# Performance work log

Hardware: AMD Instinct MI355X
Metric: run time of the kernel (lower is better)

## Reference

```python
import jax, jax.numpy as jnp
import numpy as np

N_NODES = 100000
F_IN = 128


def gcn_conv(x, W, b, src, dst, num_nodes):
    """PyG GCNConv: add self-loops, symmetric deg^-1/2 normalization,
    aggregate then linear (equivalently linear then aggregate)."""
    h = x @ W  # [N, F_out]
    # self-loops
    loop = jnp.arange(num_nodes, dtype=src.dtype)
    s = jnp.concatenate([src, loop])
    d = jnp.concatenate([dst, loop])
    ones = jnp.ones(s.shape[0], dtype=x.dtype)
    deg = jax.ops.segment_sum(ones, d, num_segments=num_nodes)  # in-degree w/ self-loops
    dinv = jnp.where(deg > 0, jax.lax.rsqrt(deg), 0.0)
    norm = dinv[s] * dinv[d]  # [E+N]
    msg = h[s] * norm[:, None]  # gather + scale
    out = jax.ops.segment_sum(msg, d, num_segments=num_nodes)  # scatter-add
    return out + b


def setup_inputs() -> dict:
    key = jax.random.key(0)
    k1, k2, k3, k4 = jax.random.split(key, 4)
    x = jax.random.normal(k1, (N_NODES, F_IN), dtype=jnp.float32)
    edge_index = jax.random.randint(k2, (2, 600000), 0, N_NODES, dtype=jnp.int64)
    # GCNConv weights (glorot-ish scale) and zero biases
    W1 = jax.random.normal(k3, (F_IN, F_IN), dtype=jnp.float32) / np.sqrt(F_IN)
    b1 = jnp.zeros((F_IN,), dtype=jnp.float32)
    W2 = jax.random.normal(k4, (F_IN, 2 * F_IN), dtype=jnp.float32) / np.sqrt(F_IN)
    b2 = jnp.zeros((2 * F_IN,), dtype=jnp.float32)
    return {"x": x, "edge_index": edge_index, "W1": W1, "b1": b1, "W2": W2, "b2": b2}


def reference(x, edge_index, W1, b1, W2, b2):
    src, dst = edge_index[0], edge_index[1]
    n = x.shape[0]
    h = gcn_conv(x, W1, b1, src, dst, n)
    h = jax.nn.relu(h)  # dropout is identity in eval mode
    h = gcn_conv(h, W2, b2, src, dst, n)
    h = jax.nn.relu(h)
    return jnp.mean(h, axis=0)  # [2*F_IN]
```

## Files before the change

### kernel.cpp

```cpp
#include <hip/hip_runtime.h>


typedef __attribute__((ext_vector_type(8))) short short8;
typedef __attribute__((ext_vector_type(4))) float f32x4;

__device__ __forceinline__ float b2f(unsigned short u) {
    union { unsigned int i; float f; } c;
    c.i = ((unsigned int)u) << 16;
    return c.f;
}
__device__ __forceinline__ unsigned short f2b(float x) {
    union { float f; unsigned int i; } c;
    c.f = x;
    unsigned int r = c.i + 0x7FFFu + ((c.i >> 16) & 1u);
    return (unsigned short)(r >> 16);
}

__device__ __forceinline__ int edge_idx(const void* ei, int is64, int which,
                                        int E, int e) {
    if (is64) return (int)((const long long*)ei)[(size_t)which * E + e];
    return ((const int*)ei)[(size_t)which * E + e];
}

__global__ void k_init(const int* __restrict__ ei, int E, int* __restrict__ counts,
                       int* __restrict__ flag, int N) {
    int i = blockIdx.x * 256 + threadIdx.x;
    if (i < N) counts[i] = 0;
    if (blockIdx.x == 0) {
        __shared__ int anyv[4];
        int t = threadIdx.x;
        int v = 0;
#pragma unroll
        for (int r = 0; r < 4; ++r) {
            long long k = (long long)(t * 4 + r) * E >> 10;
            v |= ei[2 * (int)k + 1];
        }
        unsigned long long m = __ballot(v != 0);
        if ((t & 63) == 0) anyv[t >> 6] = (m != 0ull) ? 1 : 0;
        __syncthreads();
        if (t == 0) flag[0] = anyv[0] | anyv[1] | anyv[2] | anyv[3];
    }
}

__global__ void k_count(const void* __restrict__ ei, const int* __restrict__ flag,
                        int* __restrict__ counts, int E) {
    int e = blockIdx.x * 256 + threadIdx.x;
    if (e >= E) return;
    int is64 = (*flag == 0);
    int d = edge_idx(ei, is64, 1, E, e);
    atomicAdd(&counts[d], 1);
}

__global__ void k_scan1(const int* __restrict__ counts, int* __restrict__ offs,
                        int* __restrict__ blockSums, float* __restrict__ dinv,
                        int n) {
    __shared__ int tmp[256];
    int t = threadIdx.x;
    int i = blockIdx.x * 256 + t;
    int my = (i < n) ? counts[i] : 0;
    if (i < n) dinv[i] = rsqrtf(1.0f + (float)my);
    tmp[t] = my;
    __syncthreads();
    for (int off = 1; off < 256; off <<= 1) {
        int v = (t >= off) ? tmp[t - off] : 0;
        __syncthreads();
        tmp[t] += v;
        __syncthreads();
    }
    if (i < n) offs[i] = tmp[t] - my;
    if (t == 255) blockSums[blockIdx.x] = tmp[255];
}

__global__ void k_scan2(int* __restrict__ blockSums, int nb) {
    __shared__ int tmp[512];
    __shared__ int carry;
    int t = threadIdx.x;
    if (t == 0) carry = 0;
    __syncthreads();
    for (int base = 0; base < nb; base += 512) {
        int i = base + t;
        int my = (i < nb) ? blockSums[i] : 0;
        tmp[t] = my;
        __syncthreads();
        for (int off = 1; off < 512; off <<= 1) {
            int v = (t >= off) ? tmp[t - off] : 0;
            __syncthreads();
            tmp[t] += v;
            __syncthreads();
        }
        if (i < nb) blockSums[i] = carry + tmp[t] - my;
        __syncthreads();
        if (t == 0) carry += tmp[511];
        __syncthreads();
    }
}

__global__ void k_scan3(int* __restrict__ offs, const int* __restrict__ blockSums,
                        int* __restrict__ cursor, int n) {
    int i = blockIdx.x * 256 + threadIdx.x;
    if (i < n) {
        int o = offs[i] + blockSums[blockIdx.x];
        offs[i] = o;
        cursor[i] = o;
    }
}

__global__ void k_fill_csr(const void* __restrict__ ei, const int* __restrict__ flag,
                           const float* __restrict__ dinv, int* __restrict__ cursor,
                           int2* __restrict__ csr2, int E) {
    int e = blockIdx.x * 256 + threadIdx.x;
    if (e >= E) return;
    int is64 = (*flag == 0);
    int s = edge_idx(ei, is64, 0, E, e);
    int d = edge_idx(ei, is64, 1, E, e);
    int pos = atomicAdd(&cursor[d], 1);
    csr2[pos] = make_int2(s, __float_as_int(dinv[s] * dinv[d]));
}

__global__ void k_cvt_x(const float* __restrict__ x, unsigned short* __restrict__ xb,
                        int n4) {
    int i = blockIdx.x * 256 + threadIdx.x;
    if (i >= n4) return;
    float4 v = reinterpret_cast<const float4*>(x)[i];
    ushort4 o;
    o.x = f2b(v.x); o.y = f2b(v.y); o.z = f2b(v.z); o.w = f2b(v.w);
    reinterpret_cast<ushort4*>(xb)[i] = o;
}

__global__ void k_cvt_w(const float* __restrict__ W1, const float* __restrict__ W2,
                        unsigned short* __restrict__ wt1,
                        unsigned short* __restrict__ wt2) {
    int idx = blockIdx.x * 256 + threadIdx.x;
    if (idx < 128 * 128) {
        int k = idx >> 7, n = idx & 127;
        wt1[(size_t)n * 128 + k] = f2b(W1[idx]);
    } else if (idx < 128 * 128 + 128 * 256) {
        int i2 = idx - 128 * 128;
        int k = i2 >> 8, n = i2 & 255;
        wt2[(size_t)n * 128 + k] = f2b(W2[i2]);
    }
}

template <int CHUNK>
__global__ __launch_bounds__(256) void k_gather_b(const unsigned short* __restrict__ h,
                                                  const float* __restrict__ dinv,
                                                  const int* __restrict__ offs,
                                                  const int* __restrict__ counts,
                                                  const int2* __restrict__ csr2,
                                                  unsigned short* __restrict__ g,
                                                  int N) {
    const int wid = threadIdx.x >> 6;
    const int slot = (threadIdx.x >> 4) & 3;
    const int l16 = threadIdx.x & 15;
    const short8* h8 = reinterpret_cast<const short8*>(h);
    const int start = blockIdx.x * (CHUNK * 4);

    for (int i = 0; i < CHUNK; ++i) {
        const int node = start + i * 4 + wid;
        if (node >= N) continue;
        float a[8] = {0.f, 0.f, 0.f, 0.f, 0.f, 0.f, 0.f, 0.f};
        const size_t rowu = (size_t)node * 16 + l16;
        if (slot == 0) {
            const float dd = dinv[node];
            const float w0 = dd * dd;
            short8 sv = h8[rowu];
#pragma unroll
            for (int j = 0; j < 8; ++j) a[j] = b2f((unsigned short)sv[j]) * w0;
        }
        const int beg = offs[node], cnt = counts[node];
        for (int e = slot; e < cnt; e += 4) {
            int2 p = csr2[beg + e];
            short8 v = h8[(size_t)p.x * 16 + l16];
            float w = __int_as_float(p.y);
#pragma unroll
            for (int j = 0; j < 8; ++j)
                a[j] = fmaf(b2f((unsigned short)v[j]), w, a[j]);
        }
#pragma unroll
        for (int j = 0; j < 8; ++j) {
            a[j] += __shfl_xor(a[j], 16);
            a[j] += __shfl_xor(a[j], 32);
        }
        if (slot == 0) {
            short8 o;
#pragma unroll
            for (int j = 0; j < 8; ++j) o[j] = (short)f2b(a[j]);
            reinterpret_cast<short8*>(g)[rowu] = o;
        }
    }
}

template <int KOUT, bool REDUCE, int CHUNK>
__global__ __launch_bounds__(256) void k_mgemm(const unsigned short* __restrict__ A,
                                               const unsigned short* __restrict__ WT,
                                               const float* __restrict__ bias,
                                               unsigned short* __restrict__ C,
                                               float* __restrict__ partials, int N) {
    constexpr int NFW = KOUT / 64;
    const int tid = threadIdx.x;
    const int wave = tid >> 6, lane = tid & 63;
    const int l15 = lane & 15, lg = lane >> 4;
    const int colbase = wave * (KOUT / 4);

    short8 breg[NFW][4];
    float bv[NFW];
#pragma unroll
    for (int nf = 0; nf < NFW; ++nf) {
        int col = colbase + nf * 16 + l15;
        bv[nf] = bias[col];
#pragma unroll
        for (int kk = 0; kk < 4; ++kk)
            breg[nf][kk] = *reinterpret_cast<const short8*>(
                WT + (size_t)col * 128 + kk * 32 + lg * 8);
    }

    float psum[NFW];
#pragma unroll
    for (int nf = 0; nf < NFW; ++nf) psum[nf] = 0.f;

    const int NT = (N + 15) / 16;
    const int t0 = blockIdx.x * CHUNK;
    const int tend = (t0 + CHUNK < NT) ? t0 + CHUNK : NT;

#pragma unroll 2
    for (int t = t0; t < tend; ++t) {
        const int rows = t * 16;
        const int arow = rows + l15;
        short8 a[4];
        const bool rv = arow < N;
#pragma unroll
        for (int kk = 0; kk < 4; ++kk)
            a[kk] = rv ? *reinterpret_cast<const short8*>(
                             A + (size_t)arow * 128 + kk * 32 + lg * 8)
                       : (short8){0, 0, 0, 0, 0, 0, 0, 0};

        f32x4 acc[NFW];
#pragma unroll
        for (int nf = 0; nf < NFW; ++nf) acc[nf] = (f32x4){0.f, 0.f, 0.f, 0.f};
#pragma unroll
        for (int kk = 0; kk < 4; ++kk)
#pragma unroll
            for (int nf = 0; nf < NFW; ++nf)
                acc[nf] = __builtin_amdgcn_mfma_f32_16x16x32_bf16(
                    a[kk], breg[nf][kk], acc[nf], 0, 0, 0);

        if (!REDUCE) {
#pragma unroll
            for (int nf = 0; nf < NFW; ++nf) {
                int col = colbase + nf * 16 + l15;
#pragma unroll
                for (int r = 0; r < 4; ++r) {
                    int rr = rows + lg * 4 + r;
                    if (rr < N)
                        C[(size_t)rr * KOUT + col] =
                            f2b(fmaxf(acc[nf][r] + bv[nf], 0.f));
                }
            }
        } else {
#pragma unroll
            for (int nf = 0; nf < NFW; ++nf) {
#pragma unroll
                for (int r = 0; r < 4; ++r) {
                    int rr = rows + lg * 4 + r;
                    if (rr < N) psum[nf] += fmaxf(acc[nf][r] + bv[nf], 0.f);
                }
            }
        }
    }

    if (REDUCE) {
#pragma unroll
        for (int nf = 0; nf < NFW; ++nf) {
            float s = psum[nf];
            s += __shfl_xor(s, 16);
            s += __shfl_xor(s, 32);
            if (lg == 0)
                partials[(size_t)blockIdx.x * KOUT + colbase + nf * 16 + l15] = s;
        }
    }
}

__global__ void k_reduce1(const float* __restrict__ partials, float* __restrict__ p2,
                          int NB) {
    int c = threadIdx.x;
    float sum = 0.f;
    for (int r = blockIdx.x; r < NB; r += 16)
        sum += partials[(size_t)r * 256 + c];
    p2[blockIdx.x * 256 + c] = sum;
}

__global__ void k_reduce2(const float* __restrict__ p2, float* __restrict__ out,
                          float invN) {
    int c = threadIdx.x;
    float sum = 0.f;
#pragma unroll
    for (int b = 0; b < 16; ++b) sum += p2[b * 256 + c];
    out[c] = sum * invN;
}

extern "C" void kernel_launch(void* const* d_in, const int* in_sizes, int n_in,
                              void* d_out, int out_size, void* d_ws, size_t ws_size,
                              hipStream_t stream) {
    const float* x  = (const float*)d_in[0];
    const void*  ei = d_in[1];
    const float* W1 = (const float*)d_in[2];
    const float* b1 = (const float*)d_in[3];
    const float* W2 = (const float*)d_in[4];
    const float* b2 = (const float*)d_in[5];
    float* out = (float*)d_out;

    const int N = in_sizes[0] / 128;
    const int E = in_sizes[1] / 2;
    const int nb = (N + 255) / 256;
    constexpr int GCHUNK = 4;
    constexpr int MCHUNK = 8;
    const int NT = (N + 15) / 16;
    const int NBLK = (NT + MCHUNK - 1) / MCHUNK;
    const int GBLK = (N + GCHUNK * 4 - 1) / (GCHUNK * 4);

    char* ws = (char*)d_ws;
    size_t off = 0;
    auto alloc = [&](size_t bytes) {
        char* p = ws + off;
        off += (bytes + 255) & ~(size_t)255;
        return p;
    };
    int*            flag      = (int*)alloc(4);
    int*            counts    = (int*)alloc((size_t)N * 4);
    int*            offs      = (int*)alloc((size_t)N * 4);
    int*            cursor    = (int*)alloc((size_t)N * 4);
    int*            blockSums = (int*)alloc((size_t)nb * 4);
    float*          dinv      = (float*)alloc((size_t)N * 4);
    int2*           csr2      = (int2*)alloc((size_t)E * 8);
    float*          partials  = (float*)alloc((size_t)NBLK * 256 * 4);
    float*          p2        = (float*)alloc((size_t)16 * 256 * 4);
    unsigned short* wt1       = (unsigned short*)alloc((size_t)128 * 128 * 2);
    unsigned short* wt2       = (unsigned short*)alloc((size_t)256 * 128 * 2);
    unsigned short* xb        = (unsigned short*)alloc((size_t)N * 128 * 2);
    unsigned short* g1        = (unsigned short*)alloc((size_t)N * 128 * 2);
    unsigned short* a1r       = (unsigned short*)alloc((size_t)N * 128 * 2);
    unsigned short* g2        = xb;

    k_init<<<nb, 256, 0, stream>>>((const int*)ei, E, counts, flag, N);
    k_count<<<(E + 255) / 256, 256, 0, stream>>>(ei, flag, counts, E);
    k_scan1<<<nb, 256, 0, stream>>>(counts, offs, blockSums, dinv, N);
    k_scan2<<<1, 512, 0, stream>>>(blockSums, nb);
    k_scan3<<<nb, 256, 0, stream>>>(offs, blockSums, cursor, N);
    k_fill_csr<<<(E + 255) / 256, 256, 0, stream>>>(ei, flag, dinv, cursor, csr2, E);

    k_cvt_x<<<(N * 32 + 255) / 256, 256, 0, stream>>>(x, xb, N * 32);
    k_cvt_w<<<(128 * 384 + 255) / 256, 256, 0, stream>>>(W1, W2, wt1, wt2);

    k_gather_b<GCHUNK><<<GBLK, 256, 0, stream>>>(xb, dinv, offs, counts, csr2, g1, N);
    k_mgemm<128, false, MCHUNK><<<NBLK, 256, 0, stream>>>(g1, wt1, b1, a1r, nullptr, N);

    k_gather_b<GCHUNK><<<GBLK, 256, 0, stream>>>(a1r, dinv, offs, counts, csr2, g2, N);
    k_mgemm<256, true, MCHUNK><<<NBLK, 256, 0, stream>>>(g2, wt2, b2, nullptr, partials, N);
    k_reduce1<<<16, 256, 0, stream>>>(partials, p2, NBLK);
    k_reduce2<<<1, 256, 0, stream>>>(p2, out, 1.0f / (float)N);
}
```

Baseline: 240.1 us.

## Restructure gather so each 16-lane group streams a contiguous node range with prefetch

```diff
diff --git a/kernel.cpp b/kernel.cpp
--- a/kernel.cpp
+++ b/kernel.cpp
@@ -142,50 +142,55 @@
 }
 
 template <int CHUNK>
-__global__ __launch_bounds__(256) void k_gather_b(const unsigned short* __restrict__ h,
+__global__ __launch_bounds__(256) void k_gather_s(const unsigned short* __restrict__ h,
                                                   const float* __restrict__ dinv,
                                                   const int* __restrict__ offs,
                                                   const int* __restrict__ counts,
                                                   const int2* __restrict__ csr2,
                                                   unsigned short* __restrict__ g,
-                                                  int N) {
-    const int wid = threadIdx.x >> 6;
-    const int slot = (threadIdx.x >> 4) & 3;
-    const int l16 = threadIdx.x & 15;
+                                                  int N, int E) {
+    const int grp = threadIdx.x >> 4, l16 = threadIdx.x & 15;
     const short8* h8 = reinterpret_cast<const short8*>(h);
-    const int start = blockIdx.x * (CHUNK * 4);
-
-    for (int i = 0; i < CHUNK; ++i) {
-        const int node = start + i * 4 + wid;
-        if (node >= N) continue;
-        float a[8] = {0.f, 0.f, 0.f, 0.f, 0.f, 0.f, 0.f, 0.f};
-        const size_t rowu = (size_t)node * 16 + l16;
-        if (slot == 0) {
-            const float dd = dinv[node];
+    int n = (blockIdx.x * 16 + grp) * CHUNK;
+    if (n >= N) return;
+    const int gend = (n + CHUNK < N) ? n + CHUNK : N;
+    int e = offs[n];
+    int eEnd = e + counts[n];
+    const int endAll = (gend < N) ? offs[gend] : E;
+
+    float dd = dinv[n];
+    short8 selfv = h8[(size_t)n * 16 + l16];
+    float a[8] = {0.f, 0.f, 0.f, 0.f, 0.f, 0.f, 0.f, 0.f};
+
+    int2 p = make_int2(0, 0);
+    short8 v = (short8){0, 0, 0, 0, 0, 0, 0, 0};
+    if (e < endAll) { p = csr2[e]; v = h8[(size_t)p.x * 16 + l16]; }
+
+    for (;;) {
+        if (e == eEnd) {
             const float w0 = dd * dd;
-            short8 sv = h8[rowu];
-#pragma unroll
-            for (int j = 0; j < 8; ++j) a[j] = b2f((unsigned short)sv[j]) * w0;
-        }
-        const int beg = offs[node], cnt = counts[node];
-        for (int e = slot; e < cnt; e += 4) {
-            int2 p = csr2[beg + e];
-            short8 v = h8[(size_t)p.x * 16 + l16];
-            float w = __int_as_float(p.y);
+            short8 o;
+#pragma unroll
+            for (int j = 0; j < 8; ++j) {
+                float t = fmaf(b2f((unsigned short)selfv[j]), w0, a[j]);
+                o[j] = (short)f2b(t);
+            }
+            reinterpret_cast<short8*>(g)[(size_t)n * 16 + l16] = o;
+            if (++n == gend) break;
+            dd = dinv[n];
+            selfv = h8[(size_t)n * 16 + l16];
+            eEnd += counts[n];
+#pragma unroll
+            for (int j = 0; j < 8; ++j) a[j] = 0.f;
+        } else {
+            const int en = e + 1;
+            int2 pn = p; short8 vn = v;
+            if (en < endAll) { pn = csr2[en]; vn = h8[(size_t)pn.x * 16 + l16]; }
+            const float w = __int_as_float(p.y);
 #pragma unroll
             for (int j = 0; j < 8; ++j)
                 a[j] = fmaf(b2f((unsigned short)v[j]), w, a[j]);
-        }
-#pragma unroll
-        for (int j = 0; j < 8; ++j) {
-            a[j] += __shfl_xor(a[j], 16);
-            a[j] += __shfl_xor(a[j], 32);
-        }
-        if (slot == 0) {
-            short8 o;
-#pragma unroll
-            for (int j = 0; j < 8; ++j) o[j] = (short)f2b(a[j]);
-            reinterpret_cast<short8*>(g)[rowu] = o;
+            p = pn; v = vn; e = en;
         }
     }
 }
@@ -316,7 +321,7 @@
     constexpr int MCHUNK = 8;
     const int NT = (N + 15) / 16;
     const int NBLK = (NT + MCHUNK - 1) / MCHUNK;
-    const int GBLK = (N + GCHUNK * 4 - 1) / (GCHUNK * 4);
+    const int GBLK = (N + GCHUNK * 16 - 1) / (GCHUNK * 16);
 
     char* ws = (char*)d_ws;
     size_t off = 0;
@@ -351,10 +356,10 @@
     k_cvt_x<<<(N * 32 + 255) / 256, 256, 0, stream>>>(x, xb, N * 32);
     k_cvt_w<<<(128 * 384 + 255) / 256, 256, 0, stream>>>(W1, W2, wt1, wt2);
 
-    k_gather_b<GCHUNK><<<GBLK, 256, 0, stream>>>(xb, dinv, offs, counts, csr2, g1, N);
+    k_gather_s<GCHUNK><<<GBLK, 256, 0, stream>>>(xb, dinv, offs, counts, csr2, g1, N, E);
     k_mgemm<128, false, MCHUNK><<<NBLK, 256, 0, stream>>>(g1, wt1, b1, a1r, nullptr, N);
 
-    k_gather_b<GCHUNK><<<GBLK, 256, 0, stream>>>(a1r, dinv, offs, counts, csr2, g2, N);
+    k_gather_s<GCHUNK><<<GBLK, 256, 0, stream>>>(a1r, dinv, offs, counts, csr2, g2, N, E);
     k_mgemm<256, true, MCHUNK><<<NBLK, 256, 0, stream>>>(g2, wt2, b2, nullptr, partials, N);
     k_reduce1<<<16, 256, 0, stream>>>(partials, p2, NBLK);
     k_reduce2<<<1, 256, 0, stream>>>(p2, out, 1.0f / (float)N);
```

Measured after the change: 233.3 us. 1.03x faster.

## Fuse neighbor aggregation into MFMA GEMM via swizzled LDS tiles

Applied to the files above, without the earlier changes.

```diff
diff --git a/kernel.cpp b/kernel.cpp
--- a/kernel.cpp
+++ b/kernel.cpp
@@ -141,61 +141,17 @@
     }
 }
 
-template <int CHUNK>
-__global__ __launch_bounds__(256) void k_gather_b(const unsigned short* __restrict__ h,
-                                                  const float* __restrict__ dinv,
-                                                  const int* __restrict__ offs,
-                                                  const int* __restrict__ counts,
-                                                  const int2* __restrict__ csr2,
-                                                  unsigned short* __restrict__ g,
-                                                  int N) {
-    const int wid = threadIdx.x >> 6;
-    const int slot = (threadIdx.x >> 4) & 3;
-    const int l16 = threadIdx.x & 15;
-    const short8* h8 = reinterpret_cast<const short8*>(h);
-    const int start = blockIdx.x * (CHUNK * 4);
-
-    for (int i = 0; i < CHUNK; ++i) {
-        const int node = start + i * 4 + wid;
-        if (node >= N) continue;
-        float a[8] = {0.f, 0.f, 0.f, 0.f, 0.f, 0.f, 0.f, 0.f};
-        const size_t rowu = (size_t)node * 16 + l16;
-        if (slot == 0) {
-            const float dd = dinv[node];
-            const float w0 = dd * dd;
-            short8 sv = h8[rowu];
-#pragma unroll
-            for (int j = 0; j < 8; ++j) a[j] = b2f((unsigned short)sv[j]) * w0;
-        }
-        const int beg = offs[node], cnt = counts[node];
-        for (int e = slot; e < cnt; e += 4) {
-            int2 p = csr2[beg + e];
-            short8 v = h8[(size_t)p.x * 16 + l16];
-            float w = __int_as_float(p.y);
-#pragma unroll
-            for (int j = 0; j < 8; ++j)
-                a[j] = fmaf(b2f((unsigned short)v[j]), w, a[j]);
-        }
-#pragma unroll
-        for (int j = 0; j < 8; ++j) {
-            a[j] += __shfl_xor(a[j], 16);
-            a[j] += __shfl_xor(a[j], 32);
-        }
-        if (slot == 0) {
-            short8 o;
-#pragma unroll
-            for (int j = 0; j < 8; ++j) o[j] = (short)f2b(a[j]);
-            reinterpret_cast<short8*>(g)[rowu] = o;
-        }
-    }
-}
-
-template <int KOUT, bool REDUCE, int CHUNK>
-__global__ __launch_bounds__(256) void k_mgemm(const unsigned short* __restrict__ A,
+template <int KOUT, bool REDUCE>
+__global__ __launch_bounds__(256) void k_fused(const unsigned short* __restrict__ h,
+                                               const float* __restrict__ dinv,
+                                               const int* __restrict__ offs,
+                                               const int* __restrict__ counts,
+                                               const int2* __restrict__ csr2,
                                                const unsigned short* __restrict__ WT,
                                                const float* __restrict__ bias,
                                                unsigned short* __restrict__ C,
                                                float* __restrict__ partials, int N) {
+    __shared__ unsigned short rowsm[64 * 128];
     constexpr int NFW = KOUT / 64;
     const int tid = threadIdx.x;
     const int wave = tid >> 6, lane = tid & 63;
@@ -214,25 +170,60 @@
                 WT + (size_t)col * 128 + kk * 32 + lg * 8);
     }
 
+    {
+        const int grp = tid >> 4, l16 = tid & 15;
+        const short8* h8 = reinterpret_cast<const short8*>(h);
+        const int nbase = blockIdx.x * 64 + grp;
+        for (int i = 0; i < 4; ++i) {
+            const int node = nbase + i * 16;
+            if (node < N) {
+                const float dd = dinv[node];
+                const float w0 = dd * dd;
+                short8 sv = h8[(size_t)node * 16 + l16];
+                float a[8];
+#pragma unroll
+                for (int j = 0; j < 8; ++j) a[j] = b2f((unsigned short)sv[j]) * w0;
+                const int beg = offs[node], cnt = counts[node];
+                if (cnt > 0) {
+                    int2 p = csr2[beg];
+                    short8 v = h8[(size_t)p.x * 16 + l16];
+                    for (int e = 1; e < cnt; ++e) {
+                        int2 pn = csr2[beg + e];
+                        short8 vn = h8[(size_t)pn.x * 16 + l16];
+                        float w = __int_as_float(p.y);
+#pragma unroll
+                        for (int j = 0; j < 8; ++j)
+                            a[j] = fmaf(b2f((unsigned short)v[j]), w, a[j]);
+                        p = pn; v = vn;
+                    }
+                    float w = __int_as_float(p.y);
+#pragma unroll
+                    for (int j = 0; j < 8; ++j)
+                        a[j] = fmaf(b2f((unsigned short)v[j]), w, a[j]);
+                }
+                short8 o;
+#pragma unroll
+                for (int j = 0; j < 8; ++j) o[j] = (short)f2b(a[j]);
+                const int r = grp + i * 16;
+                *reinterpret_cast<short8*>(
+                    &rowsm[r * 128 + ((l16 * 8) ^ ((r & 7) << 3))]) = o;
+            }
+        }
+    }
+    __syncthreads();
+
     float psum[NFW];
 #pragma unroll
     for (int nf = 0; nf < NFW; ++nf) psum[nf] = 0.f;
 
-    const int NT = (N + 15) / 16;
-    const int t0 = blockIdx.x * CHUNK;
-    const int tend = (t0 + CHUNK < NT) ? t0 + CHUNK : NT;
-
-#pragma unroll 2
-    for (int t = t0; t < tend; ++t) {
-        const int rows = t * 16;
-        const int arow = rows + l15;
+#pragma unroll
+    for (int t = 0; t < 4; ++t) {
+        const int r = t * 16 + l15;
         short8 a[4];
-        const bool rv = arow < N;
 #pragma unroll
         for (int kk = 0; kk < 4; ++kk)
-            a[kk] = rv ? *reinterpret_cast<const short8*>(
-                             A + (size_t)arow * 128 + kk * 32 + lg * 8)
-                       : (short8){0, 0, 0, 0, 0, 0, 0, 0};
+            a[kk] = *reinterpret_cast<const short8*>(
+                &rowsm[r * 128 + (((kk * 4 + lg) * 8) ^ ((r & 7) << 3))]);
 
         f32x4 acc[NFW];
 #pragma unroll
@@ -244,25 +235,26 @@
                 acc[nf] = __builtin_amdgcn_mfma_f32_16x16x32_bf16(
                     a[kk], breg[nf][kk], acc[nf], 0, 0, 0);
 
+        const int orow = blockIdx.x * 64 + t * 16 + lg * 4;
         if (!REDUCE) {
 #pragma unroll
             for (int nf = 0; nf < NFW; ++nf) {
                 int col = colbase + nf * 16 + l15;
 #pragma unroll
-                for (int r = 0; r < 4; ++r) {
-                    int rr = rows + lg * 4 + r;
+                for (int r2 = 0; r2 < 4; ++r2) {
+                    int rr = orow + r2;
                     if (rr < N)
                         C[(size_t)rr * KOUT + col] =
-                            f2b(fmaxf(acc[nf][r] + bv[nf], 0.f));
+                            f2b(fmaxf(acc[nf][r2] + bv[nf], 0.f));
                 }
             }
         } else {
 #pragma unroll
             for (int nf = 0; nf < NFW; ++nf) {
 #pragma unroll
-                for (int r = 0; r < 4; ++r) {
-                    int rr = rows + lg * 4 + r;
-                    if (rr < N) psum[nf] += fmaxf(acc[nf][r] + bv[nf], 0.f);
+                for (int r2 = 0; r2 < 4; ++r2) {
+                    int rr = orow + r2;
+                    if (rr < N) psum[nf] += fmaxf(acc[nf][r2] + bv[nf], 0.f);
                 }
             }
         }
@@ -312,11 +304,7 @@
     const int N = in_sizes[0] / 128;
     const int E = in_sizes[1] / 2;
     const int nb = (N + 255) / 256;
-    constexpr int GCHUNK = 4;
-    constexpr int MCHUNK = 8;
-    const int NT = (N + 15) / 16;
-    const int NBLK = (NT + MCHUNK - 1) / MCHUNK;
-    const int GBLK = (N + GCHUNK * 4 - 1) / (GCHUNK * 4);
+    const int FBLK = (N + 63) / 64;
 
     char* ws = (char*)d_ws;
     size_t off = 0;
@@ -332,14 +320,12 @@
     int*            blockSums = (int*)alloc((size_t)nb * 4);
     float*          dinv      = (float*)alloc((size_t)N * 4);
     int2*           csr2      = (int2*)alloc((size_t)E * 8);
-    float*          partials  = (float*)alloc((size_t)NBLK * 256 * 4);
+    float*          partials  = (float*)alloc((size_t)FBLK * 256 * 4);
     float*          p2        = (float*)alloc((size_t)16 * 256 * 4);
     unsigned short* wt1       = (unsigned short*)alloc((size_t)128 * 128 * 2);
     unsigned short* wt2       = (unsigned short*)alloc((size_t)256 * 128 * 2);
     unsigned short* xb        = (unsigned short*)alloc((size_t)N * 128 * 2);
-    unsigned short* g1        = (unsigned short*)alloc((size_t)N * 128 * 2);
     unsigned short* a1r       = (unsigned short*)alloc((size_t)N * 128 * 2);
-    unsigned short* g2        = xb;
 
     k_init<<<nb, 256, 0, stream>>>((const int*)ei, E, counts, flag, N);
     k_count<<<(E + 255) / 256, 256, 0, stream>>>(ei, flag, counts, E);
@@ -351,11 +337,11 @@
     k_cvt_x<<<(N * 32 + 255) / 256, 256, 0, stream>>>(x, xb, N * 32);
     k_cvt_w<<<(128 * 384 + 255) / 256, 256, 0, stream>>>(W1, W2, wt1, wt2);
 
-    k_gather_b<GCHUNK><<<GBLK, 256, 0, stream>>>(xb, dinv, offs, counts, csr2, g1, N);
-    k_mgemm<128, false, MCHUNK><<<NBLK, 256, 0, stream>>>(g1, wt1, b1, a1r, nullptr, N);
-
-    k_gather_b<GCHUNK><<<GBLK, 256, 0, stream>>>(a1r, dinv, offs, counts, csr2, g2, N);
-    k_mgemm<256, true, MCHUNK><<<NBLK, 256, 0, stream>>>(g2, wt2, b2, nullptr, partials, N);
-    k_reduce1<<<16, 256, 0, stream>>>(partials, p2, NBLK);
+    k_fused<128, false><<<FBLK, 256, 0, stream>>>(xb, dinv, offs, counts, csr2,
+                                                  wt1, b1, a1r, nullptr, N);
+
+    k_fused<256, true><<<FBLK, 256, 0, stream>>>(a1r, dinv, offs, counts, csr2,
+                                                 wt2, b2, nullptr, partials, N);
+    k_reduce1<<<16, 256, 0, stream>>>(partials, p2, FBLK);
     k_reduce2<<<1, 256, 0, stream>>>(p2, out, 1.0f / (float)N);
 }
```

After: 230.6 us. 4.0% less time.

## Assign one 16-lane group per node in gather with software-pipelined edge loads

Applied to the files above, without the earlier changes.

```diff
diff --git a/kernel.cpp b/kernel.cpp
--- a/kernel.cpp
+++ b/kernel.cpp
@@ -149,44 +149,43 @@
                                                   const int2* __restrict__ csr2,
                                                   unsigned short* __restrict__ g,
                                                   int N) {
-    const int wid = threadIdx.x >> 6;
-    const int slot = (threadIdx.x >> 4) & 3;
-    const int l16 = threadIdx.x & 15;
+    const int grp = threadIdx.x >> 4, l16 = threadIdx.x & 15;
     const short8* h8 = reinterpret_cast<const short8*>(h);
-    const int start = blockIdx.x * (CHUNK * 4);
+    const int base = blockIdx.x * (CHUNK * 16) + grp;
 
     for (int i = 0; i < CHUNK; ++i) {
-        const int node = start + i * 4 + wid;
-        if (node >= N) continue;
-        float a[8] = {0.f, 0.f, 0.f, 0.f, 0.f, 0.f, 0.f, 0.f};
+        const int node = base + i * 16;
+        if (node >= N) break;
+        const float dd = dinv[node];
+        const float w0 = dd * dd;
         const size_t rowu = (size_t)node * 16 + l16;
-        if (slot == 0) {
-            const float dd = dinv[node];
-            const float w0 = dd * dd;
-            short8 sv = h8[rowu];
-#pragma unroll
-            for (int j = 0; j < 8; ++j) a[j] = b2f((unsigned short)sv[j]) * w0;
-        }
+        short8 sv = h8[rowu];
+        float a[8];
+#pragma unroll
+        for (int j = 0; j < 8; ++j) a[j] = b2f((unsigned short)sv[j]) * w0;
+
         const int beg = offs[node], cnt = counts[node];
-        for (int e = slot; e < cnt; e += 4) {
-            int2 p = csr2[beg + e];
-            short8 v = h8[(size_t)p.x * 16 + l16];
-            float w = __int_as_float(p.y);
-#pragma unroll
-            for (int j = 0; j < 8; ++j)
-                a[j] = fmaf(b2f((unsigned short)v[j]), w, a[j]);
-        }
-#pragma unroll
-        for (int j = 0; j < 8; ++j) {
-            a[j] += __shfl_xor(a[j], 16);
-            a[j] += __shfl_xor(a[j], 32);
-        }
-        if (slot == 0) {
-            short8 o;
-#pragma unroll
-            for (int j = 0; j < 8; ++j) o[j] = (short)f2b(a[j]);
-            reinterpret_cast<short8*>(g)[rowu] = o;
-        }
+        if (cnt > 0) {
+            const int last = beg + cnt - 1;
+            int i1 = beg + 1 <= last ? beg + 1 : last;
+            int2 p0 = csr2[beg], p1 = csr2[i1];
+            short8 v0 = h8[(size_t)p0.x * 16 + l16];
+            short8 v1 = h8[(size_t)p1.x * 16 + l16];
+            for (int e = 0; e < cnt; ++e) {
+                int inx = beg + e + 2 <= last ? beg + e + 2 : last;
+                int2 pn = csr2[inx];
+                short8 vn = h8[(size_t)pn.x * 16 + l16];
+                float w = __int_as_float(p0.y);
+#pragma unroll
+                for (int j = 0; j < 8; ++j)
+                    a[j] = fmaf(b2f((unsigned short)v0[j]), w, a[j]);
+                p0 = p1; v0 = v1; p1 = pn; v1 = vn;
+            }
+        }
+        short8 o;
+#pragma unroll
+        for (int j = 0; j < 8; ++j) o[j] = (short)f2b(a[j]);
+        reinterpret_cast<short8*>(g)[rowu] = o;
     }
 }
 
@@ -312,11 +311,11 @@
     const int N = in_sizes[0] / 128;
     const int E = in_sizes[1] / 2;
     const int nb = (N + 255) / 256;
-    constexpr int GCHUNK = 4;
-    constexpr int MCHUNK = 8;
+    constexpr int GCHUNK = 2;
+    constexpr int MCHUNK = 4;
     const int NT = (N + 15) / 16;
     const int NBLK = (NT + MCHUNK - 1) / MCHUNK;
-    const int GBLK = (N + GCHUNK * 4 - 1) / (GCHUNK * 4);
+    const int GBLK = (N + GCHUNK * 16 - 1) / (GCHUNK * 16);
 
     char* ws = (char*)d_ws;
     size_t off = 0;
```

Result: slower. 249.7 us (+4.0%).
